# Optimization experiments

Hardware: AMD Instinct MI355X
Metric: run time of the kernel (lower is better)

## Reference

```python
import jax, jax.numpy as jnp
import numpy as np

ENT_TOTAL = 1_000_000
REL_TOTAL = 10_000
HIDDEN = 128      # == ent_size == rel_size
REL_TYPE = 1_000
MARGIN = 1.0
BATCH = 8192


def setup_inputs() -> dict:
    key = jax.random.key(0)
    ks = jax.random.split(key, 10)
    return {
        "ent_emb": jax.random.normal(ks[0], (ENT_TOTAL, HIDDEN), jnp.float32) * 0.05,
        "rel_emb": jax.random.normal(ks[1], (REL_TOTAL, HIDDEN), jnp.float32) * 0.05,
        "type_mat": jax.random.normal(ks[2], (REL_TYPE, HIDDEN * HIDDEN), jnp.float32) * 0.05,
        "pos_h": jax.random.randint(ks[3], (BATCH,), 0, ENT_TOTAL, jnp.int64 if jax.config.jax_enable_x64 else jnp.int32),
        "pos_t": jax.random.randint(ks[4], (BATCH,), 0, ENT_TOTAL, jnp.int32),
        "pos_r": jax.random.randint(ks[5], (BATCH,), 0, REL_TOTAL, jnp.int32),
        "pos_type_r": jax.random.randint(ks[6], (BATCH,), 0, REL_TYPE, jnp.int32),
        "neg_h": jax.random.randint(ks[7], (BATCH,), 0, ENT_TOTAL, jnp.int32),
        "neg_t": jax.random.randint(ks[8], (BATCH,), 0, ENT_TOTAL, jnp.int32),
        "neg_r": jax.random.randint(ks[9], (BATCH,), 0, REL_TOTAL, jnp.int32),
    }


def _l2norm(x):
    return x * jax.lax.rsqrt(jnp.sum(x * x, axis=-1, keepdims=True) + 1e-12)


def _calc(h, t, r):
    # l2-normalize each, then |h + r - t|
    return jnp.abs(_l2norm(h) + _l2norm(r) - _l2norm(t))


def reference(ent_emb, rel_emb, type_mat, pos_h, pos_t, pos_r, pos_type_r,
              neg_h, neg_t, neg_r):
    B = pos_h.shape[0]
    D = ent_emb.shape[1]
    # gathers
    p_h = ent_emb[pos_h]                       # [B, D]
    p_t = ent_emb[pos_t]
    p_r = rel_emb[pos_r]
    n_h = ent_emb[neg_h]
    n_t = ent_emb[neg_t]
    n_r = rel_emb[neg_r]
    # per-sample transfer matrix; original code uses pos_type_r for BOTH
    # positive and negative (faithful to source).
    T = type_mat[pos_type_r].reshape(B, D, D)  # [B, ent_size, rel_size]
    # per-sample transfer: [B, D] x [B, D, R] -> [B, R]
    p_h_ = jnp.einsum('bd,bdr->br', p_h, T)
    p_t_ = jnp.einsum('bd,bdr->br', p_t, T)
    n_h_ = jnp.einsum('bd,bdr->br', n_h, T)
    n_t_ = jnp.einsum('bd,bdr->br', n_t, T)
    p_score = jnp.sum(_calc(p_h_, p_t_, p_r), axis=-1, keepdims=True)  # [B,1]
    n_score = jnp.sum(_calc(n_h_, n_t_, n_r), axis=-1, keepdims=True)
    loss = jnp.mean(jnp.maximum(p_score - n_score + MARGIN, 0.0))
    return loss
```

## Files before the change

### kernel.cpp

```cpp
#include <hip/hip_runtime.h>

#define D 128
#define CHUNK 64
#define MAX_TYPES 1024
#define MAX_B 8192
#define MARGIN 1.0f

#define WS_NITEMS 0
#define WS_ORDER  64
#define WS_ITEMS  8448
#define WS_NEEDED ((size_t)(WS_ITEMS + 4 * 2048) * 4)


__global__ __launch_bounds__(1024) void group_kernel(
    const int* __restrict__ type_r, int* __restrict__ ws,
    float* __restrict__ out, int B, int ntype)
{
    __shared__ int hist[MAX_TYPES];
    __shared__ int typec[MAX_B];
    __shared__ int wsum[16], wsum2[16];
    const int tid = threadIdx.x;
    const int lane = tid & 63;
    const int wv = tid >> 6;

    if (tid == 0) out[0] = 0.0f;
    hist[tid] = 0;
    __syncthreads();

    const int B4 = B >> 2;
    const int4* t4p = (const int4*)type_r;
    for (int i = tid; i < B4; i += 1024) {
        const int4 t = t4p[i];
        typec[i * 4 + 0] = t.x; atomicAdd(&hist[t.x], 1);
        typec[i * 4 + 1] = t.y; atomicAdd(&hist[t.y], 1);
        typec[i * 4 + 2] = t.z; atomicAdd(&hist[t.z], 1);
        typec[i * 4 + 3] = t.w; atomicAdd(&hist[t.w], 1);
    }
    for (int i = (B4 << 2) + tid; i < B; i += 1024) {
        const int t = type_r[i];
        typec[i] = t;
        atomicAdd(&hist[t], 1);
    }
    __syncthreads();

    const int c  = (tid < ntype) ? hist[tid] : 0;
    const int ic = (c + CHUNK - 1) / CHUNK;
    int vc = c, vic = ic;
    #pragma unroll
    for (int off = 1; off < 64; off <<= 1) {
        const int tc  = __shfl_up(vc,  off);
        const int tic = __shfl_up(vic, off);
        if (lane >= off) { vc += tc; vic += tic; }
    }
    if (lane == 63) { wsum[wv] = vc; wsum2[wv] = vic; }
    __syncthreads();
    if (wv == 0 && lane < 16) {
        int a = wsum[lane], b = wsum2[lane];
        #pragma unroll
        for (int off = 1; off < 16; off <<= 1) {
            const int ta = __shfl_up(a, off);
            const int tb = __shfl_up(b, off);
            if (lane >= off) { a += ta; b += tb; }
        }
        wsum[lane] = a; wsum2[lane] = b;
    }
    __syncthreads();
    const int base_c  = (wv ? wsum[wv - 1]  : 0) + vc - c;
    const int base_ic = (wv ? wsum2[wv - 1] : 0) + vic - ic;
    hist[tid] = base_c;
    if (tid < ntype && ic > 0) {
        int4* items = (int4*)(ws + WS_ITEMS);
        for (int k = 0; k < ic; ++k)
            items[base_ic + k] = make_int4(tid, base_c + k * CHUNK,
                                           min(CHUNK, c - k * CHUNK), 0);
    }
    if (tid == 0) ws[WS_NITEMS] = wsum2[15];
    __syncthreads();
    for (int i = tid; i < B; i += 1024) {
        const int p = atomicAdd(&hist[typec[i]], 1);
        ws[WS_ORDER + p] = i;
    }
}


#define BFLY5(x) { x += __shfl_xor(x, 1); x += __shfl_xor(x, 2); x += __shfl_xor(x, 4); \
                   x += __shfl_xor(x, 8); x += __shfl_xor(x, 16); }

#define FMA4(A, T, S) { (A).x = fmaf((T).x, (S), (A).x); (A).y = fmaf((T).y, (S), (A).y); \
                        (A).z = fmaf((T).z, (S), (A).z); (A).w = fmaf((T).w, (S), (A).w); }

struct SampleRegs {
    float2 e0, e1, e2, e3;
    float4 rp, rn;
};

__device__ __forceinline__ void fetch_sample(
    SampleRegs& S, int o,
    const float* __restrict__ ent, const float* __restrict__ rel,
    const int* __restrict__ pos_h, const int* __restrict__ pos_t,
    const int* __restrict__ pos_r, const int* __restrict__ neg_h,
    const int* __restrict__ neg_t, const int* __restrict__ neg_r,
    int l, int cg)
{
    const size_t b0 = (size_t)pos_h[o] * D;
    const size_t b1 = (size_t)pos_t[o] * D;
    const size_t b2 = (size_t)neg_h[o] * D;
    const size_t b3 = (size_t)neg_t[o] * D;
    const size_t r0 = (size_t)pos_r[o] * D;
    const size_t r1 = (size_t)neg_r[o] * D;
    S.e0 = *(const float2*)&ent[b0 + 2 * l];
    S.e1 = *(const float2*)&ent[b1 + 2 * l];
    S.e2 = *(const float2*)&ent[b2 + 2 * l];
    S.e3 = *(const float2*)&ent[b3 + 2 * l];
    S.rp = *(const float4*)&rel[r0 + 4 * cg];
    S.rn = *(const float4*)&rel[r1 + 4 * cg];
}

__device__ __forceinline__ void commit_sample(float* vbw, const SampleRegs& S, int l) {
    *(float2*)&vbw[0 * D + 2 * l] = S.e0;
    *(float2*)&vbw[1 * D + 2 * l] = S.e1;
    *(float2*)&vbw[2 * D + 2 * l] = S.e2;
    *(float2*)&vbw[3 * D + 2 * l] = S.e3;
}

__device__ __forceinline__ float sample_score(
    const float* __restrict__ T_lds, const float* __restrict__ vbw,
    int h, int cg, float4 rp, float4 rn)
{
    const float4* __restrict__ T4 = (const float4*)T_lds;
    const float4* __restrict__ vv = (const float4*)vbw;
    float4 a0 = make_float4(0.f, 0.f, 0.f, 0.f), a1 = a0, a2 = a0, a3 = a0;
    const int rb  = h * 64;
    const int vb0 = h * 16;
    #pragma unroll 4
    for (int dg = 0; dg < 16; ++dg) {
        const int row = rb + dg * 4;
        const float4 t0 = T4[(row + 0) * 32 + cg];
        const float4 t1 = T4[(row + 1) * 32 + cg];
        const float4 t2 = T4[(row + 2) * 32 + cg];
        const float4 t3 = T4[(row + 3) * 32 + cg];
        const int vi = vb0 + dg;
        const float4 v0 = vv[0 * 32 + vi];
        FMA4(a0, t0, v0.x); FMA4(a0, t1, v0.y); FMA4(a0, t2, v0.z); FMA4(a0, t3, v0.w);
        const float4 v1 = vv[1 * 32 + vi];
        FMA4(a1, t0, v1.x); FMA4(a1, t1, v1.y); FMA4(a1, t2, v1.z); FMA4(a1, t3, v1.w);
        const float4 v2 = vv[2 * 32 + vi];
        FMA4(a2, t0, v2.x); FMA4(a2, t1, v2.y); FMA4(a2, t2, v2.z); FMA4(a2, t3, v2.w);
        const float4 v3 = vv[3 * 32 + vi];
        FMA4(a3, t0, v3.x); FMA4(a3, t1, v3.y); FMA4(a3, t2, v3.z); FMA4(a3, t3, v3.w);
    }
    a0.x += __shfl_xor(a0.x, 32); a0.y += __shfl_xor(a0.y, 32);
    a0.z += __shfl_xor(a0.z, 32); a0.w += __shfl_xor(a0.w, 32);
    a1.x += __shfl_xor(a1.x, 32); a1.y += __shfl_xor(a1.y, 32);
    a1.z += __shfl_xor(a1.z, 32); a1.w += __shfl_xor(a1.w, 32);
    a2.x += __shfl_xor(a2.x, 32); a2.y += __shfl_xor(a2.y, 32);
    a2.z += __shfl_xor(a2.z, 32); a2.w += __shfl_xor(a2.w, 32);
    a3.x += __shfl_xor(a3.x, 32); a3.y += __shfl_xor(a3.y, 32);
    a3.z += __shfl_xor(a3.z, 32); a3.w += __shfl_xor(a3.w, 32);

    float sph = a0.x*a0.x + a0.y*a0.y + a0.z*a0.z + a0.w*a0.w;
    float spt = a1.x*a1.x + a1.y*a1.y + a1.z*a1.z + a1.w*a1.w;
    float snh = a2.x*a2.x + a2.y*a2.y + a2.z*a2.z + a2.w*a2.w;
    float snt = a3.x*a3.x + a3.y*a3.y + a3.z*a3.z + a3.w*a3.w;
    float spr = rp.x*rp.x + rp.y*rp.y + rp.z*rp.z + rp.w*rp.w;
    float snr = rn.x*rn.x + rn.y*rn.y + rn.z*rn.z + rn.w*rn.w;
    BFLY5(sph); BFLY5(spt); BFLY5(snh); BFLY5(snt); BFLY5(spr); BFLY5(snr);
    const float iph = rsqrtf(sph + 1e-12f);
    const float ipt = rsqrtf(spt + 1e-12f);
    const float inh = rsqrtf(snh + 1e-12f);
    const float itn = rsqrtf(snt + 1e-12f);
    const float ipr = rsqrtf(spr + 1e-12f);
    const float inr = rsqrtf(snr + 1e-12f);
    float z = fabsf(a0.x*iph + rp.x*ipr - a1.x*ipt)
            + fabsf(a0.y*iph + rp.y*ipr - a1.y*ipt)
            + fabsf(a0.z*iph + rp.z*ipr - a1.z*ipt)
            + fabsf(a0.w*iph + rp.w*ipr - a1.w*ipt)
            - fabsf(a2.x*inh + rn.x*inr - a3.x*itn)
            - fabsf(a2.y*inh + rn.y*inr - a3.y*itn)
            - fabsf(a2.z*inh + rn.z*inr - a3.z*itn)
            - fabsf(a2.w*inh + rn.w*inr - a3.w*itn);
    BFLY5(z);
    return fmaxf(z + MARGIN, 0.f);
}

__global__ __launch_bounds__(512, 4) void fused_kernel(
    const float* __restrict__ ent,
    const float* __restrict__ rel,
    const float* __restrict__ tmat,
    const int* __restrict__ pos_h,
    const int* __restrict__ pos_t,
    const int* __restrict__ pos_r,
    const int* __restrict__ neg_h,
    const int* __restrict__ neg_t,
    const int* __restrict__ neg_r,
    const int* __restrict__ ws,
    float* __restrict__ out,
    float inv_B)
{
    const int nit = ws[WS_NITEMS];
    if (blockIdx.x >= nit) return;
    const int4 item = ((const int4*)(ws + WS_ITEMS))[blockIdx.x];
    const int type  = item.x;
    const int start = item.y;
    const int cnt   = item.z;

    const int tid = threadIdx.x;
    const int l   = tid & 63;
    const int w   = tid >> 6;
    const int cg  = l & 31;
    const int h   = l >> 5;

    __shared__ float T_lds[D * D];
    __shared__ float vbuf[8][4][D];

    const int* ordr = ws + WS_ORDER;

    SampleRegs A, Bq;
    int j = w;
    const bool active = (j < cnt);
    if (active)
        fetch_sample(A, ordr[start + j], ent, rel, pos_h, pos_t, pos_r,
                     neg_h, neg_t, neg_r, l, cg);

    {
        const float4* Tg = (const float4*)(tmat + (size_t)type * (D * D));
        float4* Ts = (float4*)T_lds;
        #pragma unroll
        for (int k = 0; k < 8; ++k)
            Ts[tid + k * 512] = Tg[tid + k * 512];
    }
    __syncthreads();

    float* vbw = &vbuf[w][0][0];
    float wl = 0.f;

    if (active) {
        for (;;) {
            commit_sample(vbw, A, l);
            const int jn = j + 8;
            const bool more = jn < cnt;
            if (more)
                fetch_sample(Bq, ordr[start + jn], ent, rel, pos_h, pos_t, pos_r,
                             neg_h, neg_t, neg_r, l, cg);
            wl += sample_score(T_lds, vbw, h, cg, A.rp, A.rn);
            if (!more) break;
            j = jn; A = Bq;
        }
    }

    if (l == 0) vbuf[w][0][0] = wl;
    __syncthreads();
    if (tid == 0) {
        float s = 0.f;
        #pragma unroll
        for (int k = 0; k < 8; ++k) s += vbuf[k][0][0];
        atomicAdd(out, s * inv_B);
    }
}


__global__ __launch_bounds__(128) void transr_fallback(
    const float* __restrict__ ent, const float* __restrict__ rel,
    const float* __restrict__ tmat,
    const int* __restrict__ pos_h, const int* __restrict__ pos_t,
    const int* __restrict__ pos_r, const int* __restrict__ pos_type_r,
    const int* __restrict__ neg_h, const int* __restrict__ neg_t,
    const int* __restrict__ neg_r, float* __restrict__ out, int B)
{
    const int b = blockIdx.x;
    const int r = threadIdx.x;
    const int lane = r & 63;
    const int wid = r >> 6;
    __shared__ float4 vcomb[D];
    __shared__ float sred[16];
    vcomb[r] = make_float4(ent[(size_t)pos_h[b]*D + r], ent[(size_t)pos_t[b]*D + r],
                           ent[(size_t)neg_h[b]*D + r], ent[(size_t)neg_t[b]*D + r]);
    const float prr = rel[(size_t)pos_r[b] * D + r];
    const float nrr = rel[(size_t)neg_r[b] * D + r];
    __syncthreads();
    const float* __restrict__ T = tmat + (size_t)pos_type_r[b] * (D * D);
    float aph = 0.f, apt = 0.f, anh = 0.f, ant = 0.f;
    #pragma unroll 8
    for (int d = 0; d < D; ++d) {
        const float t = T[d * D + r];
        const float4 v = vcomb[d];
        aph = fmaf(v.x, t, aph); apt = fmaf(v.y, t, apt);
        anh = fmaf(v.z, t, anh); ant = fmaf(v.w, t, ant);
    }
    float s0 = aph*aph, s1 = apt*apt, s2 = anh*anh, s3 = ant*ant;
    float s4 = prr*prr, s5 = nrr*nrr;
    #pragma unroll
    for (int off = 32; off; off >>= 1) {
        s0 += __shfl_xor(s0, off); s1 += __shfl_xor(s1, off);
        s2 += __shfl_xor(s2, off); s3 += __shfl_xor(s3, off);
        s4 += __shfl_xor(s4, off); s5 += __shfl_xor(s5, off);
    }
    if (lane == 0) {
        sred[wid*8+0]=s0; sred[wid*8+1]=s1; sred[wid*8+2]=s2;
        sred[wid*8+3]=s3; sred[wid*8+4]=s4; sred[wid*8+5]=s5;
    }
    __syncthreads();
    const float iph = rsqrtf(sred[0]+sred[8] +1e-12f);
    const float ipt = rsqrtf(sred[1]+sred[9] +1e-12f);
    const float inh = rsqrtf(sred[2]+sred[10]+1e-12f);
    const float itn = rsqrtf(sred[3]+sred[11]+1e-12f);
    const float ipr = rsqrtf(sred[4]+sred[12]+1e-12f);
    const float inr = rsqrtf(sred[5]+sred[13]+1e-12f);
    float pterm = fabsf(aph*iph + prr*ipr - apt*ipt);
    float nterm = fabsf(anh*inh + nrr*inr - ant*itn);
    #pragma unroll
    for (int off = 32; off; off >>= 1) {
        pterm += __shfl_xor(pterm, off);
        nterm += __shfl_xor(nterm, off);
    }
    __syncthreads();
    if (lane == 0) { sred[wid*2+0] = pterm; sred[wid*2+1] = nterm; }
    __syncthreads();
    if (r == 0)
        atomicAdd(out, fmaxf(sred[0]+sred[2] - sred[1]-sred[3] + MARGIN, 0.f) / (float)B);
}


extern "C" void kernel_launch(void* const* d_in, const int* in_sizes, int n_in,
                              void* d_out, int out_size, void* d_ws, size_t ws_size,
                              hipStream_t stream) {
    const float* ent  = (const float*)d_in[0];
    const float* rel  = (const float*)d_in[1];
    const float* tmat = (const float*)d_in[2];
    const int* pos_h      = (const int*)d_in[3];
    const int* pos_t      = (const int*)d_in[4];
    const int* pos_r      = (const int*)d_in[5];
    const int* pos_type_r = (const int*)d_in[6];
    const int* neg_h      = (const int*)d_in[7];
    const int* neg_t      = (const int*)d_in[8];
    const int* neg_r      = (const int*)d_in[9];
    float* out = (float*)d_out;
    const int B = in_sizes[3];
    const int ntype = in_sizes[2] / (D * D);

    if (ws_size < WS_NEEDED || ntype > MAX_TYPES || B > MAX_B) {
        hipMemsetAsync(out, 0, sizeof(float), stream);
        transr_fallback<<<B, 128, 0, stream>>>(
            ent, rel, tmat, pos_h, pos_t, pos_r, pos_type_r,
            neg_h, neg_t, neg_r, out, B);
        return;
    }

    int* ws = (int*)d_ws;
    group_kernel<<<1, 1024, 0, stream>>>(pos_type_r, ws, out, B, ntype);
    fused_kernel<<<1280, 512, 0, stream>>>(
        ent, rel, tmat, pos_h, pos_t, pos_r, neg_h, neg_t, neg_r,
        ws, out, 1.0f / (float)B);
}
```

Baseline: 48.05 us.

## Drop separate grouping kernel; each block scans type list for its own type

Removes the single-block histogram/scatter grouping kernel and launches one block per relation type. Each block reads all B type indices, counts and compacts matching samples via a block-wide prefix scan, and processes them in rounds of 64. The aim is to remove the serial single-block pre-pass and the kernel-to-kernel dependency, with the T matrix load overlapped with the scan. In exchange, every block redundantly scans the whole type array, and per-type load is unbalanced because there is no chunking across blocks.

```diff
diff --git a/kernel.cpp b/kernel.cpp
--- a/kernel.cpp
+++ b/kernel.cpp
@@ -1,86 +1,8 @@
 #include <hip/hip_runtime.h>
 
 #define D 128
-#define CHUNK 64
-#define MAX_TYPES 1024
 #define MAX_B 8192
 #define MARGIN 1.0f
-
-#define WS_NITEMS 0
-#define WS_ORDER  64
-#define WS_ITEMS  8448
-#define WS_NEEDED ((size_t)(WS_ITEMS + 4 * 2048) * 4)
-
-
-__global__ __launch_bounds__(1024) void group_kernel(
-    const int* __restrict__ type_r, int* __restrict__ ws,
-    float* __restrict__ out, int B, int ntype)
-{
-    __shared__ int hist[MAX_TYPES];
-    __shared__ int typec[MAX_B];
-    __shared__ int wsum[16], wsum2[16];
-    const int tid = threadIdx.x;
-    const int lane = tid & 63;
-    const int wv = tid >> 6;
-
-    if (tid == 0) out[0] = 0.0f;
-    hist[tid] = 0;
-    __syncthreads();
-
-    const int B4 = B >> 2;
-    const int4* t4p = (const int4*)type_r;
-    for (int i = tid; i < B4; i += 1024) {
-        const int4 t = t4p[i];
-        typec[i * 4 + 0] = t.x; atomicAdd(&hist[t.x], 1);
-        typec[i * 4 + 1] = t.y; atomicAdd(&hist[t.y], 1);
-        typec[i * 4 + 2] = t.z; atomicAdd(&hist[t.z], 1);
-        typec[i * 4 + 3] = t.w; atomicAdd(&hist[t.w], 1);
-    }
-    for (int i = (B4 << 2) + tid; i < B; i += 1024) {
-        const int t = type_r[i];
-        typec[i] = t;
-        atomicAdd(&hist[t], 1);
-    }
-    __syncthreads();
-
-    const int c  = (tid < ntype) ? hist[tid] : 0;
-    const int ic = (c + CHUNK - 1) / CHUNK;
-    int vc = c, vic = ic;
-    #pragma unroll
-    for (int off = 1; off < 64; off <<= 1) {
-        const int tc  = __shfl_up(vc,  off);
-        const int tic = __shfl_up(vic, off);
-        if (lane >= off) { vc += tc; vic += tic; }
-    }
-    if (lane == 63) { wsum[wv] = vc; wsum2[wv] = vic; }
-    __syncthreads();
-    if (wv == 0 && lane < 16) {
-        int a = wsum[lane], b = wsum2[lane];
-        #pragma unroll
-        for (int off = 1; off < 16; off <<= 1) {
-            const int ta = __shfl_up(a, off);
-            const int tb = __shfl_up(b, off);
-            if (lane >= off) { a += ta; b += tb; }
-        }
-        wsum[lane] = a; wsum2[lane] = b;
-    }
-    __syncthreads();
-    const int base_c  = (wv ? wsum[wv - 1]  : 0) + vc - c;
-    const int base_ic = (wv ? wsum2[wv - 1] : 0) + vic - ic;
-    hist[tid] = base_c;
-    if (tid < ntype && ic > 0) {
-        int4* items = (int4*)(ws + WS_ITEMS);
-        for (int k = 0; k < ic; ++k)
-            items[base_ic + k] = make_int4(tid, base_c + k * CHUNK,
-                                           min(CHUNK, c - k * CHUNK), 0);
-    }
-    if (tid == 0) ws[WS_NITEMS] = wsum2[15];
-    __syncthreads();
-    for (int i = tid; i < B; i += 1024) {
-        const int p = atomicAdd(&hist[typec[i]], 1);
-        ws[WS_ORDER + p] = i;
-    }
-}
 
 
 #define BFLY5(x) { x += __shfl_xor(x, 1); x += __shfl_xor(x, 2); x += __shfl_xor(x, 4); \
@@ -190,20 +112,14 @@
     const int* __restrict__ pos_h,
     const int* __restrict__ pos_t,
     const int* __restrict__ pos_r,
+    const int* __restrict__ type_r,
     const int* __restrict__ neg_h,
     const int* __restrict__ neg_t,
     const int* __restrict__ neg_r,
-    const int* __restrict__ ws,
     float* __restrict__ out,
-    float inv_B)
+    int B, float inv_B)
 {
-    const int nit = ws[WS_NITEMS];
-    if (blockIdx.x >= nit) return;
-    const int4 item = ((const int4*)(ws + WS_ITEMS))[blockIdx.x];
-    const int type  = item.x;
-    const int start = item.y;
-    const int cnt   = item.z;
-
+    const int t   = blockIdx.x;
     const int tid = threadIdx.x;
     const int l   = tid & 63;
     const int w   = tid >> 6;
@@ -212,49 +128,114 @@
 
     __shared__ float T_lds[D * D];
     __shared__ float vbuf[8][4][D];
-
-    const int* ordr = ws + WS_ORDER;
-
-    SampleRegs A, Bq;
-    int j = w;
-    const bool active = (j < cnt);
-    if (active)
-        fetch_sample(A, ordr[start + j], ent, rel, pos_h, pos_t, pos_r,
-                     neg_h, neg_t, neg_r, l, cg);
-
+    int* lsc = (int*)&vbuf[0][0][0];
+
+    float4 ts[8];
     {
-        const float4* Tg = (const float4*)(tmat + (size_t)type * (D * D));
+        const float4* Tg = (const float4*)(tmat + (size_t)t * (D * D));
+        #pragma unroll
+        for (int k = 0; k < 8; ++k)
+            ts[k] = Tg[tid + k * 512];
+    }
+
+    const int per = (B + 511) >> 9;
+    int vals[16];
+    const int base = tid * per;
+    int mc = 0;
+    if (per == 16 && base + 15 < B) {
+        const int4* vp = (const int4*)(type_r + base);
+        #pragma unroll
+        for (int k = 0; k < 4; ++k) {
+            const int4 v = vp[k];
+            vals[4*k+0] = v.x; vals[4*k+1] = v.y;
+            vals[4*k+2] = v.z; vals[4*k+3] = v.w;
+        }
+    } else {
+        for (int j = 0; j < 16; ++j) {
+            const int s = base + j;
+            vals[j] = (j < per && s < B) ? type_r[s] : -1;
+        }
+    }
+    #pragma unroll
+    for (int j = 0; j < 16; ++j) mc += (vals[j] == t);
+
+    {
         float4* Ts = (float4*)T_lds;
         #pragma unroll
         for (int k = 0; k < 8; ++k)
-            Ts[tid + k * 512] = Tg[tid + k * 512];
-    }
-    __syncthreads();
-
-    float* vbw = &vbuf[w][0][0];
+            Ts[tid + k * 512] = ts[k];
+    }
+
+    int inc = mc;
+    #pragma unroll
+    for (int off = 1; off < 64; off <<= 1) {
+        const int tv = __shfl_up(inc, off);
+        if (l >= off) inc += tv;
+    }
+    if (l == 63) lsc[64 + w] = inc;
+    __syncthreads();
+    int wbase = 0, cnt = 0;
+    #pragma unroll
+    for (int k = 0; k < 8; ++k) {
+        const int s = lsc[64 + k];
+        wbase += (k < w) ? s : 0;
+        cnt += s;
+    }
+    const int excl = wbase + inc - mc;
+    __syncthreads();
+
     float wl = 0.f;
-
-    if (active) {
-        for (;;) {
-            commit_sample(vbw, A, l);
-            const int jn = j + 8;
-            const bool more = jn < cnt;
-            if (more)
-                fetch_sample(Bq, ordr[start + jn], ent, rel, pos_h, pos_t, pos_r,
-                             neg_h, neg_t, neg_r, l, cg);
-            wl += sample_score(T_lds, vbw, h, cg, A.rp, A.rn);
-            if (!more) break;
-            j = jn; A = Bq;
-        }
-    }
-
-    if (l == 0) vbuf[w][0][0] = wl;
+    for (int r0 = 0;; r0 += 64) {
+        {
+            int g = excl;
+            #pragma unroll
+            for (int j = 0; j < 16; ++j) {
+                if (vals[j] == t) {
+                    const int wr = g - r0;
+                    if (wr >= 0 && wr < 64) lsc[wr] = base + j;
+                    ++g;
+                }
+            }
+        }
+        __syncthreads();
+        const int wcnt = min(cnt - r0, 64);
+        int sidx[8];
+        int nk = 0;
+        #pragma unroll
+        for (int k = 0; k < 8; ++k) {
+            const int rank = w + 8 * k;
+            if (rank < wcnt) sidx[nk++] = lsc[rank];
+        }
+        __syncthreads();
+
+        if (nk > 0) {
+            float* vbw = &vbuf[w][0][0];
+            SampleRegs A, Bq;
+            fetch_sample(A, sidx[0], ent, rel, pos_h, pos_t, pos_r,
+                         neg_h, neg_t, neg_r, l, cg);
+            for (int k = 0;; ++k) {
+                commit_sample(vbw, A, l);
+                const bool more = (k + 1) < nk;
+                if (more)
+                    fetch_sample(Bq, sidx[k + 1], ent, rel, pos_h, pos_t, pos_r,
+                                 neg_h, neg_t, neg_r, l, cg);
+                wl += sample_score(T_lds, vbw, h, cg, A.rp, A.rn);
+                if (!more) break;
+                A = Bq;
+            }
+        }
+        if (r0 + 64 >= cnt) break;
+        __syncthreads();
+    }
+
+    __syncthreads();
+    if (l == 0) ((float*)lsc)[w] = wl;
     __syncthreads();
     if (tid == 0) {
         float s = 0.f;
         #pragma unroll
-        for (int k = 0; k < 8; ++k) s += vbuf[k][0][0];
-        atomicAdd(out, s * inv_B);
+        for (int k = 0; k < 8; ++k) s += ((float*)lsc)[k];
+        if (s != 0.f) atomicAdd(out, s * inv_B);
     }
 }
 
@@ -338,17 +319,16 @@
     const int B = in_sizes[3];
     const int ntype = in_sizes[2] / (D * D);
 
-    if (ws_size < WS_NEEDED || ntype > MAX_TYPES || B > MAX_B) {
-        hipMemsetAsync(out, 0, sizeof(float), stream);
+    hipMemsetAsync(out, 0, sizeof(float), stream);
+
+    if (B > MAX_B) {
         transr_fallback<<<B, 128, 0, stream>>>(
             ent, rel, tmat, pos_h, pos_t, pos_r, pos_type_r,
             neg_h, neg_t, neg_r, out, B);
         return;
     }
 
-    int* ws = (int*)d_ws;
-    group_kernel<<<1, 1024, 0, stream>>>(pos_type_r, ws, out, B, ntype);
-    fused_kernel<<<1280, 512, 0, stream>>>(
-        ent, rel, tmat, pos_h, pos_t, pos_r, neg_h, neg_t, neg_r,
-        ws, out, 1.0f / (float)B);
-}
+    fused_kernel<<<ntype, 512, 0, stream>>>(
+        ent, rel, tmat, pos_h, pos_t, pos_r, pos_type_r,
+        neg_h, neg_t, neg_r, out, B, 1.0f / (float)B);
+}
```

Measured after the change: 46.61 us. 3.0% less time.
